# Performance work log

Measured on AMD Instinct MI355X. Metric: run time of the kernel, lower is better.

The kernel has to match this reference:

```python
import jax, jax.numpy as jnp
import numpy as np
import math

QK_DIM = 128

def setup_inputs() -> dict:
    key = jax.random.key(0)
    kx, kq, kk, kv = jax.random.split(key, 4)
    B, S, D, H = 4, 4096, 1024, 128
    X = jax.random.normal(kx, (B, S, D), dtype=jnp.float32)
    # xavier-normal-ish scale for weights
    std = math.sqrt(2.0 / (D + H))
    W_q = jax.random.normal(kq, (D, H), dtype=jnp.float32) * std
    W_k = jax.random.normal(kk, (D, H), dtype=jnp.float32) * std
    W_v = jax.random.normal(kv, (D, H), dtype=jnp.float32) * std
    return {"X": X, "W_q": W_q, "W_k": W_k, "W_v": W_v}

def reference(X, W_q, W_k, W_v):
    # X: [B, S, D]; single-head causal attention
    Q = X @ W_q                       # [B, S, H]
    K = X @ W_k                       # [B, S, H]
    V = X @ W_v                       # [B, S, H]
    S_len = X.shape[1]
    scores = jnp.einsum('bsh,bth->bst', Q, K) / math.sqrt(QK_DIM)  # [B, S, S]
    causal = jnp.tril(jnp.ones((S_len, S_len), dtype=bool))
    scores = jnp.where(causal, scores, -jnp.inf)
    attn = jax.nn.softmax(scores, axis=-1)
    return jnp.einsum('bst,bth->bsh', attn, V)
```

## Files before the change

kernel.cpp:

```cpp
#include <hip/hip_runtime.h>
#include <hip/hip_bf16.h>

#define B_ 4
#define S_ 4096
#define D_ 1024
#define H_ 128

typedef unsigned short u16;
typedef unsigned int u32;
typedef short s16x8 __attribute__((ext_vector_type(8)));
typedef float f32x4 __attribute__((ext_vector_type(4)));
typedef float f32x16 __attribute__((ext_vector_type(16)));

__device__ __forceinline__ u16 f2bf(float f) {
    u32 x = __float_as_uint(f);
    u32 r = x + 0x7fffu + ((x >> 16) & 1u);
    return (u16)(r >> 16);
}

__device__ __forceinline__ u32 cvtpk_bf16(float a, float b) {
    u32 r;
    asm("v_cvt_pk_bf16_f32 %0, %1, %2" : "=v"(r) : "v"(a), "v"(b));
    return r;
}
__device__ __forceinline__ void pl32swap(u32& x, u32& y) {
    asm("v_permlane32_swap_b32 %0, %1" : "+v"(x), "+v"(y));
}

__device__ __forceinline__ void gl_lds16(const u16* g, u16* l) {
    __builtin_amdgcn_global_load_lds(
        (const __attribute__((address_space(1))) u32*)g,
        (__attribute__((address_space(3))) u32*)l, 16, 0, 0);
}

__global__ void detect_dtype_kernel(const u32* __restrict__ w, int* __restrict__ flag) {
    __shared__ int smax[256];
    const int tid = threadIdx.x;
    int m = 0;
    for (int i = tid; i < 1024; i += 256) {
        u32 x = w[i];
        m = max(m, max((int)((x >> 7) & 0xFF), (int)((x >> 23) & 0xFF)));
    }
    smax[tid] = m;
    __syncthreads();
    if (tid == 0) {
        int mm = 0;
        for (int i = 0; i < 256; ++i) mm = max(mm, smax[i]);
        *flag = (mm >= 200) ? 1 : 0;
    }
}

__global__ __launch_bounds__(256) void prep_w_kernel(
    const void* __restrict__ Wq, const void* __restrict__ Wk, const void* __restrict__ Wv,
    u16* __restrict__ Wt, const int* __restrict__ dflag)
{
    const int kt = blockIdx.x, mat = blockIdx.y;
    const void* W = (mat == 0) ? Wq : (mat == 1) ? Wk : Wv;
    const int isf = *dflag;
    const int t = threadIdx.x;
    const int kk = t >> 3;
    const int n0 = (t & 7) * 16;
    u16 vals[16];
    if (isf) {
        const float* wp = (const float*)W + (size_t)(kt * 32 + kk) * H_ + n0;
#pragma unroll
        for (int i = 0; i < 16; ++i) vals[i] = f2bf(wp[i]);
    } else {
        const u16* wp = (const u16*)W + (size_t)(kt * 32 + kk) * H_ + n0;
#pragma unroll
        for (int i = 0; i < 16; ++i) vals[i] = wp[i];
    }
    const size_t base = (size_t)(mat * 32 + kt) * 128;
#pragma unroll
    for (int i = 0; i < 16; ++i)
        Wt[(base + n0 + i) * 32 + kk] = vals[i];
}

__global__ __launch_bounds__(256) void qkv_kernel(
    const void* __restrict__ Xv, const u16* __restrict__ Wt,
    u16* __restrict__ Qo, u16* __restrict__ Ko, u16* __restrict__ Vto,
    const int* __restrict__ dflag)
{
    __shared__ u16 Ws[2][384 * 32];
    __shared__ union { u16 qk[32 * 136]; u16 vt[128 * 40]; } OsU;

    const int isf = *dflag;
    const int tid = threadIdx.x;
    const int w = tid >> 6, lane = tid & 63;
    const int r = lane & 15, q = lane >> 4;
    const size_t m0 = (size_t)blockIdx.x * 32;

    f32x4 acc[2][6];
#pragma unroll
    for (int s2 = 0; s2 < 2; ++s2)
#pragma unroll
        for (int i = 0; i < 6; ++i) acc[s2][i] = (f32x4){0.f, 0.f, 0.f, 0.f};

    const float* xf0 = (const float*)Xv + (m0 + r) * D_;
    const float* xf1 = (const float*)Xv + (m0 + 16 + r) * D_;
    const u16*   xb0 = (const u16*)Xv + (m0 + r) * D_;
    const u16*   xb1 = (const u16*)Xv + (m0 + 16 + r) * D_;

    float4 af[2][2];
    uint4  ab[2];

#pragma unroll
    for (int i = 0; i < 6; ++i) {
        int c = tid + i * 256;
        gl_lds16(Wt + (size_t)((c >> 9) * 32) * 4096 + (c & 511) * 8, &Ws[0][c * 8]);
    }
    if (isf) {
        af[0][0] = *(const float4*)(xf0 + q * 8);
        af[0][1] = *(const float4*)(xf0 + q * 8 + 4);
        af[1][0] = *(const float4*)(xf1 + q * 8);
        af[1][1] = *(const float4*)(xf1 + q * 8 + 4);
    } else {
        ab[0] = *(const uint4*)(xb0 + q * 8);
        ab[1] = *(const uint4*)(xb1 + q * 8);
    }

    for (int kt = 0; kt < 32; ++kt) {
        const int buf = kt & 1;
        __syncthreads();

        if (kt + 1 < 32) {
#pragma unroll
            for (int i = 0; i < 6; ++i) {
                int c = tid + i * 256;
                gl_lds16(Wt + (size_t)((c >> 9) * 32 + kt + 1) * 4096 + (c & 511) * 8,
                         &Ws[buf ^ 1][c * 8]);
            }
        }

        s16x8 a[2];
        if (isf) {
#pragma unroll
            for (int s2 = 0; s2 < 2; ++s2) {
                union { u16 u[8]; s16x8 v; } pk;
                pk.u[0] = f2bf(af[s2][0].x); pk.u[1] = f2bf(af[s2][0].y);
                pk.u[2] = f2bf(af[s2][0].z); pk.u[3] = f2bf(af[s2][0].w);
                pk.u[4] = f2bf(af[s2][1].x); pk.u[5] = f2bf(af[s2][1].y);
                pk.u[6] = f2bf(af[s2][1].z); pk.u[7] = f2bf(af[s2][1].w);
                a[s2] = pk.v;
            }
        } else {
            a[0] = *(const s16x8*)&ab[0];
            a[1] = *(const s16x8*)&ab[1];
        }

        if (kt + 1 < 32) {
            const int k0 = (kt + 1) * 32;
            if (isf) {
                af[0][0] = *(const float4*)(xf0 + k0 + q * 8);
                af[0][1] = *(const float4*)(xf0 + k0 + q * 8 + 4);
                af[1][0] = *(const float4*)(xf1 + k0 + q * 8);
                af[1][1] = *(const float4*)(xf1 + k0 + q * 8 + 4);
            } else {
                ab[0] = *(const uint4*)(xb0 + k0 + q * 8);
                ab[1] = *(const uint4*)(xb1 + k0 + q * 8);
            }
        }

#pragma unroll
        for (int i = 0; i < 6; ++i) {
            int c = w * 6 + i;
            s16x8 b = *(const s16x8*)&Ws[buf][(c >> 3) * 4096 + ((c & 7) * 16 + r) * 32 + q * 8];
            acc[0][i] = __builtin_amdgcn_mfma_f32_16x16x32_bf16(a[0], b, acc[0][i], 0, 0, 0);
            acc[1][i] = __builtin_amdgcn_mfma_f32_16x16x32_bf16(a[1], b, acc[1][i], 0, 0, 0);
        }
    }

    u16* outs[2] = {Qo, Ko};
    for (int m = 0; m < 2; ++m) {
        const float sc = (m == 0) ? 0.08838834764831845f : 1.0f;
        __syncthreads();
#pragma unroll
        for (int i = 0; i < 6; ++i) {
            int c = w * 6 + i;
            if ((c >> 3) == m) {
                int nt = c & 7;
#pragma unroll
                for (int s2 = 0; s2 < 2; ++s2)
#pragma unroll
                    for (int reg = 0; reg < 4; ++reg)
                        OsU.qk[(s2 * 16 + q * 4 + reg) * 136 + nt * 16 + r] = f2bf(acc[s2][i][reg] * sc);
            }
        }
        __syncthreads();
        u16* Out = outs[m];
#pragma unroll
        for (int it = 0; it < 2; ++it) {
            int c = tid + it * 256;
            int row = c >> 4, col = (c & 15) * 8;
            *(uint4*)(Out + (m0 + row) * H_ + col) = *(const uint4*)&OsU.qk[row * 136 + col];
        }
    }

    __syncthreads();
#pragma unroll
    for (int i = 0; i < 6; ++i) {
        int c = w * 6 + i;
        if ((c >> 3) == 2) {
            int nt = c & 7;
#pragma unroll
            for (int s2 = 0; s2 < 2; ++s2)
#pragma unroll
                for (int reg = 0; reg < 4; ++reg)
                    OsU.vt[(nt * 16 + r) * 40 + s2 * 16 + q * 4 + reg] = f2bf(acc[s2][i][reg]);
        }
    }
    __syncthreads();
    {
        const int bb = blockIdx.x >> 7;
        const int s0 = (blockIdx.x & 127) * 32;
#pragma unroll
        for (int it = 0; it < 2; ++it) {
            int c = tid + it * 256;
            int h = c >> 2, sh = (c & 3) * 8;
            *(uint4*)(Vto + ((size_t)bb * H_ + h) * S_ + s0 + sh) =
                *(const uint4*)&OsU.vt[h * 40 + sh];
        }
    }
}

__global__ __launch_bounds__(256) void attn_kernel(
    const u16* __restrict__ Q, const u16* __restrict__ K, const u16* __restrict__ Vt,
    void* __restrict__ out, const int* __restrict__ dflag)
{
    __shared__ float opS[4][32][128];
    __shared__ float lpS[4][32];

    const int isf = *dflag;
    const int tid = threadIdx.x;
    const int w = tid >> 6, lane = tid & 63;
    const int l31 = lane & 31, hi = lane >> 5;
    const int bid = blockIdx.x;
    const int b = bid & 3;
    const int qt = (bid < 256) ? (bid >> 2) : (127 - ((bid - 256) >> 2));

    const u16* Qg  = Q  + ((size_t)b * S_ + (size_t)qt * 32) * H_;
    const u16* Kg  = K  + (size_t)b * S_ * H_;
    const u16* Vtg = Vt + (size_t)b * H_ * S_;

    s16x8 qf[8];
#pragma unroll
    for (int sl = 0; sl < 8; ++sl)
        qf[sl] = *(const s16x8*)(Qg + (size_t)l31 * H_ + sl * 16 + hi * 8);

    f32x16 accO[4];
#pragma unroll
    for (int hg = 0; hg < 4; ++hg)
#pragma unroll
        for (int i = 0; i < 16; ++i) accO[hg][i] = 0.f;
    float lp = 0.f;

    s16x8 kf[8];
    if (w <= qt) {
#pragma unroll
        for (int sl = 0; sl < 8; ++sl)
            kf[sl] = *(const s16x8*)(Kg + ((size_t)w * 32 + l31) * H_ + sl * 16 + hi * 8);
    }

    for (int c = w; c <= qt; c += 4) {
        const int kb = c * 32;

        s16x8 vf[4][2];
#pragma unroll
        for (int hg = 0; hg < 4; ++hg)
#pragma unroll
            for (int ks = 0; ks < 2; ++ks)
                vf[hg][ks] = *(const s16x8*)(Vtg + (size_t)(hg * 32 + l31) * S_ + kb + ks * 16 + hi * 8);

        f32x16 sacc;
#pragma unroll
        for (int i = 0; i < 16; ++i) sacc[i] = 0.f;
#pragma unroll
        for (int sl = 0; sl < 8; ++sl)
            sacc = __builtin_amdgcn_mfma_f32_32x32x16_bf16(kf[sl], qf[sl], sacc, 0, 0, 0);

        if (c + 4 <= qt) {
#pragma unroll
            for (int sl = 0; sl < 8; ++sl)
                kf[sl] = *(const s16x8*)(Kg + ((size_t)(kb + 128) + l31) * H_ + sl * 16 + hi * 8);
        }

        const bool diag = (c == qt);
        float p[16];
#pragma unroll
        for (int r = 0; r < 16; ++r) {
            float s = fminf(sacc[r], 80.f);
            float pv = __expf(s);
            if (diag && ((r & 3) + 8 * (r >> 2) + 4 * hi) > l31) pv = 0.f;
            lp += pv;
            p[r] = pv;
        }

        u32 w01 = cvtpk_bf16(p[0], p[1]),  w23 = cvtpk_bf16(p[2], p[3]);
        u32 w45 = cvtpk_bf16(p[4], p[5]),  w67 = cvtpk_bf16(p[6], p[7]);
        pl32swap(w01, w45);
        pl32swap(w23, w67);
        u32 x01 = cvtpk_bf16(p[8], p[9]),  x23 = cvtpk_bf16(p[10], p[11]);
        u32 x45 = cvtpk_bf16(p[12], p[13]), x67 = cvtpk_bf16(p[14], p[15]);
        pl32swap(x01, x45);
        pl32swap(x23, x67);
        union { u32 u[4]; s16x8 v; } pa0, pa1;
        pa0.u[0] = w01; pa0.u[1] = w23; pa0.u[2] = w45; pa0.u[3] = w67;
        pa1.u[0] = x01; pa1.u[1] = x23; pa1.u[2] = x45; pa1.u[3] = x67;

#pragma unroll
        for (int hg = 0; hg < 4; ++hg) {
            accO[hg] = __builtin_amdgcn_mfma_f32_32x32x16_bf16(pa0.v, vf[hg][0], accO[hg], 0, 0, 0);
            accO[hg] = __builtin_amdgcn_mfma_f32_32x32x16_bf16(pa1.v, vf[hg][1], accO[hg], 0, 0, 0);
        }
    }

    lp += __shfl_xor(lp, 32);

#pragma unroll
    for (int hg = 0; hg < 4; ++hg)
#pragma unroll
        for (int r = 0; r < 16; ++r)
            opS[w][(r & 3) + 8 * (r >> 2) + 4 * hi][hg * 32 + l31] = accO[hg][r];
    if (lane < 32) lpS[w][l31] = lp;
    __syncthreads();

    {
        const int q = tid >> 3;
        const int hs = (tid & 7) * 16;
        const float l = lpS[0][q] + lpS[1][q] + lpS[2][q] + lpS[3][q];
        const float inv = 1.0f / l;
        float vals[16];
#pragma unroll
        for (int i = 0; i < 16; i += 4) {
            float4 a0 = *(const float4*)&opS[0][q][hs + i];
            float4 a1 = *(const float4*)&opS[1][q][hs + i];
            float4 a2 = *(const float4*)&opS[2][q][hs + i];
            float4 a3 = *(const float4*)&opS[3][q][hs + i];
            vals[i + 0] = (a0.x + a1.x + a2.x + a3.x) * inv;
            vals[i + 1] = (a0.y + a1.y + a2.y + a3.y) * inv;
            vals[i + 2] = (a0.z + a1.z + a2.z + a3.z) * inv;
            vals[i + 3] = (a0.w + a1.w + a2.w + a3.w) * inv;
        }
        const size_t orow = (size_t)b * S_ + (size_t)qt * 32 + q;
        if (isf) {
            float* dst = (float*)out + orow * H_ + hs;
#pragma unroll
            for (int i = 0; i < 4; ++i)
                *(float4*)(dst + i * 4) = *(const float4*)(&vals[i * 4]);
        } else {
            u16* dst = (u16*)out + orow * H_ + hs;
#pragma unroll
            for (int hh = 0; hh < 2; ++hh) {
                union { u16 u[8]; uint4 v; } pk;
#pragma unroll
                for (int i = 0; i < 8; ++i) pk.u[i] = f2bf(vals[hh * 8 + i]);
                *(uint4*)(dst + hh * 8) = pk.v;
            }
        }
    }
}

extern "C" void kernel_launch(void* const* d_in, const int* in_sizes, int n_in,
                              void* d_out, int out_size, void* d_ws, size_t ws_size,
                              hipStream_t stream) {
    (void)in_sizes; (void)n_in; (void)out_size; (void)ws_size;
    const void* X  = d_in[0];
    const void* Wq = d_in[1];
    const void* Wk = d_in[2];
    const void* Wv = d_in[3];

    int* dflag = (int*)d_ws;
    u16* Qw = (u16*)((char*)d_ws + 256);
    const size_t n = (size_t)B_ * S_ * H_;
    u16* Kw = Qw + n;
    u16* Vtw = Kw + n;
    u16* Wt = Vtw + n;

    detect_dtype_kernel<<<1, 256, 0, stream>>>((const u32*)Wq, dflag);
    prep_w_kernel<<<dim3(32, 3), 256, 0, stream>>>(Wq, Wk, Wv, Wt, dflag);
    qkv_kernel<<<512, 256, 0, stream>>>(X, Wt, Qw, Kw, Vtw, dflag);
    attn_kernel<<<512, 256, 0, stream>>>(Qw, Kw, Vtw, d_out, dflag);
}
```

Baseline: 207.1 us.

## Use eight waves per attention block to split key chunks further

Doubles the attention block to 512 threads so eight waves each take every eighth 32-key chunk instead of every fourth. This shortens the serial loop per wave for long causal rows. The partial outputs are combined in two phases through the existing shared buffer, with an extra barrier. The final normalization is respread over 512 threads. The cost is higher register pressure under the 512-thread launch bound and extra reduction and synchronization work.

```diff
diff --git a/kernel.cpp b/kernel.cpp
--- a/kernel.cpp
+++ b/kernel.cpp
@@ -223,12 +223,12 @@
     }
 }
 
-__global__ __launch_bounds__(256) void attn_kernel(
+__global__ __launch_bounds__(512) void attn_kernel(
     const u16* __restrict__ Q, const u16* __restrict__ K, const u16* __restrict__ Vt,
     void* __restrict__ out, const int* __restrict__ dflag)
 {
     __shared__ float opS[4][32][128];
-    __shared__ float lpS[4][32];
+    __shared__ float lpS[8][32];
 
     const int isf = *dflag;
     const int tid = threadIdx.x;
@@ -261,7 +261,7 @@
             kf[sl] = *(const s16x8*)(Kg + ((size_t)w * 32 + l31) * H_ + sl * 16 + hi * 8);
     }
 
-    for (int c = w; c <= qt; c += 4) {
+    for (int c = w; c <= qt; c += 8) {
         const int kb = c * 32;
 
         s16x8 vf[4][2];
@@ -278,10 +278,10 @@
         for (int sl = 0; sl < 8; ++sl)
             sacc = __builtin_amdgcn_mfma_f32_32x32x16_bf16(kf[sl], qf[sl], sacc, 0, 0, 0);
 
-        if (c + 4 <= qt) {
+        if (c + 8 <= qt) {
 #pragma unroll
             for (int sl = 0; sl < 8; ++sl)
-                kf[sl] = *(const s16x8*)(Kg + ((size_t)(kb + 128) + l31) * H_ + sl * 16 + hi * 8);
+                kf[sl] = *(const s16x8*)(Kg + ((size_t)(kb + 256) + l31) * H_ + sl * 16 + hi * 8);
         }
 
         const bool diag = (c == qt);
@@ -315,47 +315,55 @@
     }
 
     lp += __shfl_xor(lp, 32);
-
-#pragma unroll
-    for (int hg = 0; hg < 4; ++hg)
-#pragma unroll
-        for (int r = 0; r < 16; ++r)
-            opS[w][(r & 3) + 8 * (r >> 2) + 4 * hi][hg * 32 + l31] = accO[hg][r];
     if (lane < 32) lpS[w][l31] = lp;
+
+    if (w < 4) {
+#pragma unroll
+        for (int hg = 0; hg < 4; ++hg)
+#pragma unroll
+            for (int r = 0; r < 16; ++r)
+                opS[w][(r & 3) + 8 * (r >> 2) + 4 * hi][hg * 32 + l31] = accO[hg][r];
+    }
+    __syncthreads();
+    if (w >= 4) {
+#pragma unroll
+        for (int hg = 0; hg < 4; ++hg)
+#pragma unroll
+            for (int r = 0; r < 16; ++r)
+                opS[w - 4][(r & 3) + 8 * (r >> 2) + 4 * hi][hg * 32 + l31] += accO[hg][r];
+    }
     __syncthreads();
 
     {
-        const int q = tid >> 3;
-        const int hs = (tid & 7) * 16;
-        const float l = lpS[0][q] + lpS[1][q] + lpS[2][q] + lpS[3][q];
+        const int qrow = tid >> 4;
+        const int hs = (tid & 15) * 8;
+        float l = 0.f;
+#pragma unroll
+        for (int s = 0; s < 8; ++s) l += lpS[s][qrow];
         const float inv = 1.0f / l;
-        float vals[16];
-#pragma unroll
-        for (int i = 0; i < 16; i += 4) {
-            float4 a0 = *(const float4*)&opS[0][q][hs + i];
-            float4 a1 = *(const float4*)&opS[1][q][hs + i];
-            float4 a2 = *(const float4*)&opS[2][q][hs + i];
-            float4 a3 = *(const float4*)&opS[3][q][hs + i];
+        float vals[8];
+#pragma unroll
+        for (int i = 0; i < 8; i += 4) {
+            float4 a0 = *(const float4*)&opS[0][qrow][hs + i];
+            float4 a1 = *(const float4*)&opS[1][qrow][hs + i];
+            float4 a2 = *(const float4*)&opS[2][qrow][hs + i];
+            float4 a3 = *(const float4*)&opS[3][qrow][hs + i];
             vals[i + 0] = (a0.x + a1.x + a2.x + a3.x) * inv;
             vals[i + 1] = (a0.y + a1.y + a2.y + a3.y) * inv;
             vals[i + 2] = (a0.z + a1.z + a2.z + a3.z) * inv;
             vals[i + 3] = (a0.w + a1.w + a2.w + a3.w) * inv;
         }
-        const size_t orow = (size_t)b * S_ + (size_t)qt * 32 + q;
+        const size_t orow = (size_t)b * S_ + (size_t)qt * 32 + qrow;
         if (isf) {
             float* dst = (float*)out + orow * H_ + hs;
-#pragma unroll
-            for (int i = 0; i < 4; ++i)
-                *(float4*)(dst + i * 4) = *(const float4*)(&vals[i * 4]);
+            *(float4*)(dst) = *(const float4*)(&vals[0]);
+            *(float4*)(dst + 4) = *(const float4*)(&vals[4]);
         } else {
             u16* dst = (u16*)out + orow * H_ + hs;
-#pragma unroll
-            for (int hh = 0; hh < 2; ++hh) {
-                union { u16 u[8]; uint4 v; } pk;
-#pragma unroll
-                for (int i = 0; i < 8; ++i) pk.u[i] = f2bf(vals[hh * 8 + i]);
-                *(uint4*)(dst + hh * 8) = pk.v;
-            }
+            union { u16 u[8]; uint4 v; } pk;
+#pragma unroll
+            for (int i = 0; i < 8; ++i) pk.u[i] = f2bf(vals[i]);
+            *(uint4*)dst = pk.v;
         }
     }
 }
@@ -379,5 +387,5 @@
     detect_dtype_kernel<<<1, 256, 0, stream>>>((const u32*)Wq, dflag);
     prep_w_kernel<<<dim3(32, 3), 256, 0, stream>>>(Wq, Wk, Wv, Wt, dflag);
     qkv_kernel<<<512, 256, 0, stream>>>(X, Wt, Qw, Kw, Vtw, dflag);
-    attn_kernel<<<512, 256, 0, stream>>>(Qw, Kw, Vtw, d_out, dflag);
-}
+    attn_kernel<<<512, 512, 0, stream>>>(Qw, Kw, Vtw, d_out, dflag);
+}
```

Result: no change. 210.9 us (+1.8%).

## Pair causal query tiles with split-KV blocks, LDS-staged K/V, and combine kernel

Applied to the files above, without the earlier changes.

Attention is restructured so each 512-thread block handles 64-query tiles and stages 128-key K/V tiles into swizzled, double-buffered LDS using global-to-LDS loads. This replaces per-wave direct global loads and lets the query tiles in a block reuse K/V. Work is balanced across causal triangle positions: a block pairs a short tile with part of a long tile, and the long tiles are split across two blocks whose partial outputs and row sums are written to a workspace. A new combine kernel merges those partials, which adds an extra launch and extra global traffic in exchange for even load and better data reuse.

```diff
diff --git a/kernel.cpp b/kernel.cpp
--- a/kernel.cpp
+++ b/kernel.cpp
@@ -223,139 +223,249 @@
     }
 }
 
-__global__ __launch_bounds__(256) void attn_kernel(
+__global__ __launch_bounds__(512) void attn_pair_kernel(
     const u16* __restrict__ Q, const u16* __restrict__ K, const u16* __restrict__ Vt,
-    void* __restrict__ out, const int* __restrict__ dflag)
+    void* __restrict__ out, float* __restrict__ OP, float* __restrict__ LP,
+    const int* __restrict__ dflag)
 {
-    __shared__ float opS[4][32][128];
-    __shared__ float lpS[4][32];
+    __shared__ u16 Ks[2][128 * 128];
+    __shared__ u16 Vs[2][128 * 128];
+    __shared__ float lpS[8][32];
 
     const int isf = *dflag;
     const int tid = threadIdx.x;
     const int w = tid >> 6, lane = tid & 63;
     const int l31 = lane & 31, hi = lane >> 5;
+    const int qs = w >> 2;
+    const int kh = w & 3;
     const int bid = blockIdx.x;
     const int b = bid & 3;
-    const int qt = (bid < 256) ? (bid >> 2) : (127 - ((bid - 256) >> 2));
-
-    const u16* Qg  = Q  + ((size_t)b * S_ + (size_t)qt * 32) * H_;
+    const int p = (bid >> 2) & 31;
+    const int c = bid >> 7;
+    const int nA = (p >> 1) + 1;
+    const int m = 17 - nA;
+
     const u16* Kg  = K  + (size_t)b * S_ * H_;
     const u16* Vtg = Vt + (size_t)b * H_ * S_;
 
-    s16x8 qf[8];
-#pragma unroll
-    for (int sl = 0; sl < 8; ++sl)
-        qf[sl] = *(const s16x8*)(Qg + (size_t)l31 * H_ + sl * 16 + hi * 8);
-
-    f32x16 accO[4];
-#pragma unroll
-    for (int hg = 0; hg < 4; ++hg)
-#pragma unroll
-        for (int i = 0; i < 16; ++i) accO[hg][i] = 0.f;
-    float lp = 0.f;
-
-    s16x8 kf[8];
-    if (w <= qt) {
+    for (int seg = 0; seg < 2; ++seg) {
+        int qt, jlo, jhi;
+        bool direct;
+        if (seg == 0) {
+            if (c != 0) continue;
+            qt = p; jlo = 0; jhi = nA; direct = true;
+        } else {
+            qt = 63 - p;
+            const int nB = ((63 - p) >> 1) + 1;
+            jlo = (c == 0) ? 0 : m; jhi = (c == 0) ? m : nB; direct = false;
+        }
+        const int nT = (qt >> 1) + 1;
+        const u16* Qg = Q + ((size_t)b * S_ + (size_t)qt * 64) * H_;
+
+        s16x8 qf[8];
 #pragma unroll
         for (int sl = 0; sl < 8; ++sl)
-            kf[sl] = *(const s16x8*)(Kg + ((size_t)w * 32 + l31) * H_ + sl * 16 + hi * 8);
-    }
-
-    for (int c = w; c <= qt; c += 4) {
-        const int kb = c * 32;
-
-        s16x8 vf[4][2];
+            qf[sl] = *(const s16x8*)(Qg + (size_t)(qs * 32 + l31) * H_ + sl * 16 + hi * 8);
+
+        f32x16 accO[4];
 #pragma unroll
         for (int hg = 0; hg < 4; ++hg)
 #pragma unroll
-            for (int ks = 0; ks < 2; ++ks)
-                vf[hg][ks] = *(const s16x8*)(Vtg + (size_t)(hg * 32 + l31) * S_ + kb + ks * 16 + hi * 8);
-
-        f32x16 sacc;
-#pragma unroll
-        for (int i = 0; i < 16; ++i) sacc[i] = 0.f;
-#pragma unroll
-        for (int sl = 0; sl < 8; ++sl)
-            sacc = __builtin_amdgcn_mfma_f32_32x32x16_bf16(kf[sl], qf[sl], sacc, 0, 0, 0);
-
-        if (c + 4 <= qt) {
+            for (int i = 0; i < 16; ++i) accO[hg][i] = 0.f;
+        float lp = 0.f;
+
+        {
+            const int j0 = jlo;
+#pragma unroll
+            for (int i = 0; i < 4; ++i) {
+                int ck = tid + i * 512;
+                int row = ck >> 4;
+                int wo = ((ck & 15) * 16) ^ ((row & 7) << 4);
+                gl_lds16(Kg + ((size_t)j0 * 128 + row) * H_ + (wo >> 1), &Ks[0][ck * 8]);
+                gl_lds16(Vtg + (size_t)row * S_ + j0 * 128 + (wo >> 1), &Vs[0][ck * 8]);
+            }
+        }
+
+        for (int j = jlo; j < jhi; ++j) {
+            const int buf = (j - jlo) & 1;
+            __syncthreads();
+
+            if (j + 1 < jhi) {
+                const int jn = j + 1;
+#pragma unroll
+                for (int i = 0; i < 4; ++i) {
+                    int ck = tid + i * 512;
+                    int row = ck >> 4;
+                    int wo = ((ck & 15) * 16) ^ ((row & 7) << 4);
+                    gl_lds16(Kg + ((size_t)jn * 128 + row) * H_ + (wo >> 1), &Ks[buf ^ 1][ck * 8]);
+                    gl_lds16(Vtg + (size_t)row * S_ + jn * 128 + (wo >> 1), &Vs[buf ^ 1][ck * 8]);
+                }
+            }
+
+            const int kr = kh * 32 + l31;
+            const u16* kbase = &Ks[buf][kr * 128];
+            s16x8 kf[8];
 #pragma unroll
             for (int sl = 0; sl < 8; ++sl)
-                kf[sl] = *(const s16x8*)(Kg + ((size_t)(kb + 128) + l31) * H_ + sl * 16 + hi * 8);
-        }
-
-        const bool diag = (c == qt);
-        float p[16];
-#pragma unroll
-        for (int r = 0; r < 16; ++r) {
-            float s = fminf(sacc[r], 80.f);
-            float pv = __expf(s);
-            if (diag && ((r & 3) + 8 * (r >> 2) + 4 * hi) > l31) pv = 0.f;
-            lp += pv;
-            p[r] = pv;
-        }
-
-        u32 w01 = cvtpk_bf16(p[0], p[1]),  w23 = cvtpk_bf16(p[2], p[3]);
-        u32 w45 = cvtpk_bf16(p[4], p[5]),  w67 = cvtpk_bf16(p[6], p[7]);
-        pl32swap(w01, w45);
-        pl32swap(w23, w67);
-        u32 x01 = cvtpk_bf16(p[8], p[9]),  x23 = cvtpk_bf16(p[10], p[11]);
-        u32 x45 = cvtpk_bf16(p[12], p[13]), x67 = cvtpk_bf16(p[14], p[15]);
-        pl32swap(x01, x45);
-        pl32swap(x23, x67);
-        union { u32 u[4]; s16x8 v; } pa0, pa1;
-        pa0.u[0] = w01; pa0.u[1] = w23; pa0.u[2] = w45; pa0.u[3] = w67;
-        pa1.u[0] = x01; pa1.u[1] = x23; pa1.u[2] = x45; pa1.u[3] = x67;
-
-#pragma unroll
-        for (int hg = 0; hg < 4; ++hg) {
-            accO[hg] = __builtin_amdgcn_mfma_f32_32x32x16_bf16(pa0.v, vf[hg][0], accO[hg], 0, 0, 0);
-            accO[hg] = __builtin_amdgcn_mfma_f32_32x32x16_bf16(pa1.v, vf[hg][1], accO[hg], 0, 0, 0);
-        }
-    }
-
-    lp += __shfl_xor(lp, 32);
-
-#pragma unroll
-    for (int hg = 0; hg < 4; ++hg)
-#pragma unroll
-        for (int r = 0; r < 16; ++r)
-            opS[w][(r & 3) + 8 * (r >> 2) + 4 * hi][hg * 32 + l31] = accO[hg][r];
-    if (lane < 32) lpS[w][l31] = lp;
-    __syncthreads();
-
-    {
-        const int q = tid >> 3;
-        const int hs = (tid & 7) * 16;
-        const float l = lpS[0][q] + lpS[1][q] + lpS[2][q] + lpS[3][q];
-        const float inv = 1.0f / l;
-        float vals[16];
-#pragma unroll
-        for (int i = 0; i < 16; i += 4) {
-            float4 a0 = *(const float4*)&opS[0][q][hs + i];
-            float4 a1 = *(const float4*)&opS[1][q][hs + i];
-            float4 a2 = *(const float4*)&opS[2][q][hs + i];
-            float4 a3 = *(const float4*)&opS[3][q][hs + i];
-            vals[i + 0] = (a0.x + a1.x + a2.x + a3.x) * inv;
-            vals[i + 1] = (a0.y + a1.y + a2.y + a3.y) * inv;
-            vals[i + 2] = (a0.z + a1.z + a2.z + a3.z) * inv;
-            vals[i + 3] = (a0.w + a1.w + a2.w + a3.w) * inv;
-        }
-        const size_t orow = (size_t)b * S_ + (size_t)qt * 32 + q;
-        if (isf) {
-            float* dst = (float*)out + orow * H_ + hs;
+                kf[sl] = *(const s16x8*)&kbase[((sl * 32 + hi * 16) ^ ((kr & 7) << 4)) >> 1];
+
+            f32x16 s0, s1;
+#pragma unroll
+            for (int i = 0; i < 16; ++i) { s0[i] = 0.f; s1[i] = 0.f; }
+#pragma unroll
+            for (int sl = 0; sl < 4; ++sl) {
+                s0 = __builtin_amdgcn_mfma_f32_32x32x16_bf16(kf[sl], qf[sl], s0, 0, 0, 0);
+                s1 = __builtin_amdgcn_mfma_f32_32x32x16_bf16(kf[sl + 4], qf[sl + 4], s1, 0, 0, 0);
+            }
+
+            s16x8 vf[4][2];
+#pragma unroll
+            for (int hg = 0; hg < 4; ++hg) {
+                const int h = hg * 32 + l31;
+                const u16* vbase = &Vs[buf][h * 128];
+#pragma unroll
+                for (int ks = 0; ks < 2; ++ks)
+                    vf[hg][ks] = *(const s16x8*)&vbase[((kh * 64 + ks * 32 + hi * 16) ^ ((h & 7) << 4)) >> 1];
+            }
+
+            const bool diag = (j == nT - 1);
+            float pv16[16];
+#pragma unroll
+            for (int r = 0; r < 16; ++r) {
+                float s = fminf(s0[r] + s1[r], 80.f);
+                float pv = __expf(s);
+                int gkey = j * 128 + kh * 32 + ((r & 3) + 8 * (r >> 2) + 4 * hi);
+                int grow = qt * 64 + qs * 32 + l31;
+                if (diag && gkey > grow) pv = 0.f;
+                lp += pv;
+                pv16[r] = pv;
+            }
+
+            u32 w01 = cvtpk_bf16(pv16[0], pv16[1]),  w23 = cvtpk_bf16(pv16[2], pv16[3]);
+            u32 w45 = cvtpk_bf16(pv16[4], pv16[5]),  w67 = cvtpk_bf16(pv16[6], pv16[7]);
+            pl32swap(w01, w45);
+            pl32swap(w23, w67);
+            u32 x01 = cvtpk_bf16(pv16[8], pv16[9]),   x23 = cvtpk_bf16(pv16[10], pv16[11]);
+            u32 x45 = cvtpk_bf16(pv16[12], pv16[13]), x67 = cvtpk_bf16(pv16[14], pv16[15]);
+            pl32swap(x01, x45);
+            pl32swap(x23, x67);
+            union { u32 u[4]; s16x8 v; } pa0, pa1;
+            pa0.u[0] = w01; pa0.u[1] = w23; pa0.u[2] = w45; pa0.u[3] = w67;
+            pa1.u[0] = x01; pa1.u[1] = x23; pa1.u[2] = x45; pa1.u[3] = x67;
+
+#pragma unroll
+            for (int hg = 0; hg < 4; ++hg) {
+                accO[hg] = __builtin_amdgcn_mfma_f32_32x32x16_bf16(pa0.v, vf[hg][0], accO[hg], 0, 0, 0);
+                accO[hg] = __builtin_amdgcn_mfma_f32_32x32x16_bf16(pa1.v, vf[hg][1], accO[hg], 0, 0, 0);
+            }
+        }
+
+        lp += __shfl_xor(lp, 32);
+        if (lane < 32) lpS[w][l31] = lp;
+        __syncthreads();
+
+        float* opSf = (float*)&Ks[0][0];
+        for (int s = 0; s < 4; ++s) {
+            if (kh == s) {
+                float* dst = opSf + qs * 32 * 128;
+#pragma unroll
+                for (int hg = 0; hg < 4; ++hg)
+#pragma unroll
+                    for (int r = 0; r < 16; ++r) {
+                        int idx = ((r & 3) + 8 * (r >> 2) + 4 * hi) * 128 + hg * 32 + l31;
+                        if (s == 0) dst[idx] = accO[hg][r];
+                        else        dst[idx] += accO[hg][r];
+                    }
+            }
+            __syncthreads();
+        }
+
+        const int row = tid >> 3;
+        const int col = (tid & 7) * 16;
+        const int rq = row & 31, rs = row >> 5;
+        const float lrow = lpS[rs * 4 + 0][rq] + lpS[rs * 4 + 1][rq] +
+                           lpS[rs * 4 + 2][rq] + lpS[rs * 4 + 3][rq];
+        const float* src = opSf + (rs * 32 + rq) * 128 + col;
+
+        if (direct) {
+            const float inv = 1.0f / lrow;
+            const size_t orow = (size_t)b * S_ + (size_t)qt * 64 + row;
+            if (isf) {
+                float* dst = (float*)out + orow * H_ + col;
+#pragma unroll
+                for (int i = 0; i < 4; ++i) {
+                    float4 v = *(const float4*)(src + i * 4);
+                    v.x *= inv; v.y *= inv; v.z *= inv; v.w *= inv;
+                    *(float4*)(dst + i * 4) = v;
+                }
+            } else {
+                u16* dst = (u16*)out + orow * H_ + col;
+#pragma unroll
+                for (int hh = 0; hh < 2; ++hh) {
+                    union { u16 u[8]; uint4 v; } pk;
+#pragma unroll
+                    for (int i = 0; i < 8; ++i) pk.u[i] = f2bf(src[hh * 8 + i] * inv);
+                    *(uint4*)(dst + hh * 8) = pk.v;
+                }
+            }
+        } else {
+            const size_t slot = (size_t)((b * 32 + p) * 2 + c);
+            float* Os = OP + slot * 64 * 128;
 #pragma unroll
             for (int i = 0; i < 4; ++i)
-                *(float4*)(dst + i * 4) = *(const float4*)(&vals[i * 4]);
-        } else {
-            u16* dst = (u16*)out + orow * H_ + hs;
-#pragma unroll
-            for (int hh = 0; hh < 2; ++hh) {
-                union { u16 u[8]; uint4 v; } pk;
-#pragma unroll
-                for (int i = 0; i < 8; ++i) pk.u[i] = f2bf(vals[hh * 8 + i]);
-                *(uint4*)(dst + hh * 8) = pk.v;
-            }
+                *(float4*)(Os + row * 128 + col + i * 4) = *(const float4*)(src + i * 4);
+            if (tid < 64)
+                LP[slot * 64 + tid] = lpS[(tid >> 5) * 4 + 0][tid & 31] + lpS[(tid >> 5) * 4 + 1][tid & 31] +
+                                      lpS[(tid >> 5) * 4 + 2][tid & 31] + lpS[(tid >> 5) * 4 + 3][tid & 31];
+        }
+        __syncthreads();
+    }
+}
+
+__global__ __launch_bounds__(256) void combine_kernel(
+    const float* __restrict__ OP, const float* __restrict__ LP,
+    void* __restrict__ out, const int* __restrict__ dflag)
+{
+    const int isf = *dflag;
+    const int bid = blockIdx.x;
+    const int b = bid >> 5;
+    const int qtl = bid & 31;
+    const int p = 31 - qtl;
+    const size_t s0 = (size_t)((b * 32 + p) * 2);
+    const int tid = threadIdx.x;
+    const int row = tid >> 2;
+    const int col0 = (tid & 3) * 32;
+
+    const float* O0 = OP + (s0 * 64 + row) * 128 + col0;
+    const float* O1 = OP + ((s0 + 1) * 64 + row) * 128 + col0;
+    const float l = LP[s0 * 64 + row] + LP[(s0 + 1) * 64 + row];
+    const float inv = 1.0f / l;
+
+    float vals[32];
+#pragma unroll
+    for (int i = 0; i < 8; ++i) {
+        float4 a = *(const float4*)(O0 + i * 4);
+        float4 bb = *(const float4*)(O1 + i * 4);
+        vals[i * 4 + 0] = (a.x + bb.x) * inv;
+        vals[i * 4 + 1] = (a.y + bb.y) * inv;
+        vals[i * 4 + 2] = (a.z + bb.z) * inv;
+        vals[i * 4 + 3] = (a.w + bb.w) * inv;
+    }
+
+    const size_t orow = (size_t)b * S_ + (size_t)(32 + qtl) * 64 + row;
+    if (isf) {
+        float* dst = (float*)out + orow * H_ + col0;
+#pragma unroll
+        for (int i = 0; i < 8; ++i)
+            *(float4*)(dst + i * 4) = *(const float4*)(&vals[i * 4]);
+    } else {
+        u16* dst = (u16*)out + orow * H_ + col0;
+#pragma unroll
+        for (int hh = 0; hh < 4; ++hh) {
+            union { u16 u[8]; uint4 v; } pk;
+#pragma unroll
+            for (int i = 0; i < 8; ++i) pk.u[i] = f2bf(vals[hh * 8 + i]);
+            *(uint4*)(dst + hh * 8) = pk.v;
         }
     }
 }
@@ -375,9 +485,12 @@
     u16* Kw = Qw + n;
     u16* Vtw = Kw + n;
     u16* Wt = Vtw + n;
+    float* OP = (float*)(Wt + 3 * 1024 * 128);
+    float* LP = OP + (size_t)256 * 64 * 128;
 
     detect_dtype_kernel<<<1, 256, 0, stream>>>((const u32*)Wq, dflag);
     prep_w_kernel<<<dim3(32, 3), 256, 0, stream>>>(Wq, Wk, Wv, Wt, dflag);
     qkv_kernel<<<512, 256, 0, stream>>>(X, Wt, Qw, Kw, Vtw, dflag);
-    attn_kernel<<<512, 256, 0, stream>>>(Qw, Kw, Vtw, d_out, dflag);
-}
+    attn_pair_kernel<<<256, 512, 0, stream>>>(Qw, Kw, Vtw, d_out, OP, LP, dflag);
+    combine_kernel<<<128, 256, 0, stream>>>(OP, LP, d_out, dflag);
+}
```

Result: faster. 191.9 us (-7.3%).
